# Performance work log

Measured on AMD Instinct MI355X. Metric: run time of the kernel, lower is better.

Reference implementation:

```python
import jax, jax.numpy as jnp
import numpy as np

N_HEAD = 8
DIM_INPUT = 1024
DIM_K = 128
DIM_V = 128
SEG = 512  # segment_length


def setup_inputs() -> dict:
    key = jax.random.key(0)
    ks = jax.random.split(key, 7)
    B, S, D = 4, 8192, DIM_INPUT
    s = 1.0 / np.sqrt(D)
    x = jax.random.normal(ks[0], (B, S, D), jnp.float32)
    wq = jax.random.normal(ks[1], (D, N_HEAD * DIM_K), jnp.float32) * s
    bq = jax.random.normal(ks[2], (N_HEAD * DIM_K,), jnp.float32) * 0.01
    wk = jax.random.normal(ks[3], (D, N_HEAD * DIM_K), jnp.float32) * s
    bk = jax.random.normal(ks[4], (N_HEAD * DIM_K,), jnp.float32) * 0.01
    wv = jax.random.normal(ks[5], (D, N_HEAD * DIM_V), jnp.float32) * s
    bv = jax.random.normal(ks[6], (N_HEAD * DIM_V,), jnp.float32) * 0.01
    beta = jnp.zeros((1,), jnp.float32)  # nn.Parameter(torch.zeros(1))
    return {"x": x, "wq": wq, "bq": bq, "wk": wk, "bk": bk, "wv": wv, "bv": bv, "beta": beta}


def reference(x, wq, bq, wk, bk, wv, bv, beta):
    B, S, D = x.shape
    nseg = S // SEG

    def proj(w, b, d):
        y = x @ w + b  # [B, S, H*d] -- one big GEMM instead of per-segment
        return y.reshape(B, nseg, SEG, N_HEAD, d).transpose(1, 0, 3, 2, 4)  # [nseg, B, H, L, d]

    q = proj(wq, bq, DIM_K)
    k = proj(wk, bk, DIM_K)
    v = proj(wv, bv, DIM_V)

    scale = 1.0 / jnp.sqrt(jnp.asarray(DIM_K, x.dtype))
    bsig = jax.nn.sigmoid(beta)  # (1,), broadcasts

    def step(carry, qkv):
        mem, z = carry  # mem: [B,H,dk,dv], z: [B,H,dk,1]
        qi, ki, vi = qkv  # [B,H,L,dk/dv]
        # memory update (before retrieval, as in source)
        sk = jax.nn.elu(ki) + 1.0
        mem = mem + jnp.einsum('bhlk,bhlv->bhkv', sk, vi)
        z = z + sk.sum(axis=2)[..., None] * SEG
        # memory retrieval
        sq = jax.nn.elu(qi) + 1.0
        a_mem = jnp.einsum('bhlk,bhkv->bhlv', sq, mem) / (
            jnp.einsum('bhlk,bhkd->bhld', sq, z) + 1e-5)
        # local softmax attention
        attn = jax.nn.softmax(jnp.einsum('bhlk,bhmk->bhlm', qi, ki) * scale, axis=-1)
        a_dot = jnp.einsum('bhlm,bhmv->bhlv', attn, vi)
        # head-mean then beta blend
        out = bsig * a_mem.mean(axis=1) + (1.0 - bsig) * a_dot.mean(axis=1)  # [B,L,dv]
        return (mem, z), out

    mem0 = jnp.zeros((B, N_HEAD, DIM_K, DIM_V), x.dtype)
    z0 = jnp.zeros((B, N_HEAD, DIM_K, 1), x.dtype)
    _, outs = jax.lax.scan(step, (mem0, z0), (q, k, v))  # outs: [nseg, B, L, dv]
    return outs.transpose(1, 0, 2, 3).reshape(B, S, DIM_V)
```

## Files before the change

### kernel.cpp

```cpp
#include <hip/hip_runtime.h>
#include <hip/hip_bf16.h>

#define B_    4
#define S_    8192
#define D_    1024
#define H_    8
#define DKV_  128
#define SEG_  512
#define NSEG_ 16
#define BS_   (B_ * S_)

typedef __attribute__((ext_vector_type(8))) short short8;
typedef __attribute__((ext_vector_type(4))) float f32x4;

__device__ inline float bf2f(unsigned short u) {
  unsigned int x = ((unsigned int)u) << 16;
  return __uint_as_float(x);
}
__device__ inline unsigned short f2bf(float f) {
  __hip_bfloat16 h = __float2bfloat16(f);
  return *(unsigned short*)&h;
}
__device__ inline void bf16split(float f, unsigned short& hi, unsigned short& lo) {
  __hip_bfloat16 h = __float2bfloat16(f);
  float hf = __bfloat162float(h);
  __hip_bfloat16 l = __float2bfloat16(f - hf);
  hi = *(unsigned short*)&h;
  lo = *(unsigned short*)&l;
}

__global__ __launch_bounds__(256) void prep_w(
    const float* __restrict__ W, __hip_bfloat16* __restrict__ Whi,
    __hip_bfloat16* __restrict__ Wlo) {
  __shared__ float tile[32][33];
  const int k0 = blockIdx.x * 32, n0 = blockIdx.y * 32;
  const int tx = threadIdx.x & 31, ty = threadIdx.x >> 5;
#pragma unroll
  for (int r = 0; r < 4; ++r) {
    int k = ty + r * 8;
    tile[k][tx] = W[(size_t)(k0 + k) * 1024 + n0 + tx];
  }
  __syncthreads();
#pragma unroll
  for (int r = 0; r < 4; ++r) {
    int n = ty + r * 8;
    float v = tile[tx][n];
    unsigned short hb, lb;
    bf16split(v, hb, lb);
    *(unsigned short*)&Whi[(size_t)(n0 + n) * 1024 + k0 + tx] = hb;
    *(unsigned short*)&Wlo[(size_t)(n0 + n) * 1024 + k0 + tx] = lb;
  }
}

template <int MODE>
__global__ __launch_bounds__(256) void gemm_bf16x3(
    const float* __restrict__ A, const __hip_bfloat16* __restrict__ Bhg,
    const __hip_bfloat16* __restrict__ Blg, const float* __restrict__ bias,
    __hip_bfloat16* __restrict__ Oh, __hip_bfloat16* __restrict__ Ol) {
  __shared__ __hip_bfloat16 Ah[128][40];
  __shared__ __hip_bfloat16 Al[128][40];
  __shared__ __hip_bfloat16 Bh[128][40];
  __shared__ __hip_bfloat16 Bl[128][40];
  const int t = threadIdx.x;
  const int m0 = blockIdx.x * 128, n0 = blockIdx.y * 128;
  const int wave = t >> 6, lane = t & 63;
  const int wm = (wave >> 1) * 64, wn = (wave & 1) * 64;
  const int lr = lane & 15, ks = lane >> 4;

  f32x4 acc[4][4];
#pragma unroll
  for (int i = 0; i < 4; ++i)
#pragma unroll
    for (int j = 0; j < 4; ++j) acc[i][j] = (f32x4){0.f, 0.f, 0.f, 0.f};

  for (int k0 = 0; k0 < 1024; k0 += 32) {
    __syncthreads();
#pragma unroll
    for (int rep = 0; rep < 4; ++rep) {
      int lin = t + rep * 256;
      int row = lin >> 3, kq = (lin & 7) * 4;
      float4 v = *(const float4*)&A[(size_t)(m0 + row) * 1024 + k0 + kq];
      ushort4 hv, lv;
      bf16split(v.x, hv.x, lv.x);
      bf16split(v.y, hv.y, lv.y);
      bf16split(v.z, hv.z, lv.z);
      bf16split(v.w, hv.w, lv.w);
      *(ushort4*)&Ah[row][kq] = hv;
      *(ushort4*)&Al[row][kq] = lv;
    }
#pragma unroll
    for (int rep = 0; rep < 2; ++rep) {
      int lin = t + rep * 256;
      int row = lin >> 2, kq = (lin & 3) * 8;
      *(uint4*)&Bh[row][kq] =
          *(const uint4*)&Bhg[(size_t)(n0 + row) * 1024 + k0 + kq];
      *(uint4*)&Bl[row][kq] =
          *(const uint4*)&Blg[(size_t)(n0 + row) * 1024 + k0 + kq];
    }
    __syncthreads();

    short8 afh[4], afl[4];
#pragma unroll
    for (int fm = 0; fm < 4; ++fm) {
      afh[fm] = *(short8*)&Ah[wm + fm * 16 + lr][ks * 8];
      afl[fm] = *(short8*)&Al[wm + fm * 16 + lr][ks * 8];
    }
#pragma unroll
    for (int fn = 0; fn < 4; ++fn) {
      short8 bfh = *(short8*)&Bh[wn + fn * 16 + lr][ks * 8];
      short8 bfl = *(short8*)&Bl[wn + fn * 16 + lr][ks * 8];
#pragma unroll
      for (int fm = 0; fm < 4; ++fm) {
        acc[fm][fn] = __builtin_amdgcn_mfma_f32_16x16x32_bf16(afh[fm], bfh, acc[fm][fn], 0, 0, 0);
        acc[fm][fn] = __builtin_amdgcn_mfma_f32_16x16x32_bf16(afh[fm], bfl, acc[fm][fn], 0, 0, 0);
        acc[fm][fn] = __builtin_amdgcn_mfma_f32_16x16x32_bf16(afl[fm], bfh, acc[fm][fn], 0, 0, 0);
      }
    }
  }
#pragma unroll
  for (int fn = 0; fn < 4; ++fn) {
    int n = n0 + wn + fn * 16 + lr;
    float bv = bias[n];
#pragma unroll
    for (int fm = 0; fm < 4; ++fm) {
      int mrow = m0 + wm + fm * 16 + ks * 4;
      if (MODE == 0) {
#pragma unroll
        for (int r = 0; r < 4; ++r) {
          float val = acc[fm][fn][r] + bv;
          unsigned short hb, lb;
          bf16split(val, hb, lb);
          *(unsigned short*)&Oh[(size_t)(mrow + r) * 1024 + n] = hb;
          *(unsigned short*)&Ol[(size_t)(mrow + r) * 1024 + n] = lb;
        }
      } else {
        int bb = mrow >> 13, s = mrow & 8191;
        size_t vtix = (((size_t)(bb * 8 + (n >> 7))) * 128 + (n & 127)) * 8192 + s;
        ushort4 pk;
        pk.x = f2bf(acc[fm][fn][0] + bv);
        pk.y = f2bf(acc[fm][fn][1] + bv);
        pk.z = f2bf(acc[fm][fn][2] + bv);
        pk.w = f2bf(acc[fm][fn][3] + bv);
        *(ushort4*)&Oh[vtix] = pk;
      }
    }
  }
}

__global__ __launch_bounds__(256) void seg_kv(
    const __hip_bfloat16* __restrict__ Khp, const __hip_bfloat16* __restrict__ Klp,
    const __hip_bfloat16* __restrict__ VTp, float* __restrict__ MemST,
    float* __restrict__ Zs) {
  __shared__ float sk[16][132];
  __shared__ float svT[128][18];
  const int bx = blockIdx.x;
  const int seg = bx >> 5, bh = bx & 31;
  const int b = bh >> 3, h = bh & 7;
  const int t = threadIdx.x;
  const int tr = t >> 4, tc = t & 15;
  float acc[8][8] = {};
  float zacc = 0.f;
  const size_t rowbase = (size_t)b * S_ + (size_t)seg * SEG_;
  const size_t sbase = (size_t)seg * SEG_;
  const size_t vtbase = (size_t)(b * 8 + h) * 128 * 8192;
  for (int l0 = 0; l0 < SEG_; l0 += 16) {
    __syncthreads();
    {
      int row = t >> 4, oct = t & 15;
      size_t g = (rowbase + l0 + row) * 1024 + h * 128 + oct * 8;
      short8 hv = *(const short8*)&Khp[g];
      short8 lv = *(const short8*)&Klp[g];
#pragma unroll
      for (int e = 0; e < 8; ++e) {
        float kvf = bf2f((unsigned short)hv[e]) + bf2f((unsigned short)lv[e]);
        sk[row][oct * 8 + e] = kvf > 0.f ? kvf + 1.f : __expf(kvf);
      }
      int dv = t >> 1, half = t & 1;
      short8 vv = *(const short8*)&VTp[vtbase + (size_t)dv * 8192 + sbase + l0 + half * 8];
#pragma unroll
      for (int e = 0; e < 8; ++e) svT[dv][half * 8 + e] = bf2f((unsigned short)vv[e]);
    }
    __syncthreads();
#pragma unroll
    for (int l = 0; l < 16; ++l) {
      float a[8], kk[8];
#pragma unroll
      for (int i = 0; i < 8; ++i) a[i] = svT[tr * 8 + i][l];
      *(float4*)&kk[0] = *(const float4*)&sk[l][tc * 8];
      *(float4*)&kk[4] = *(const float4*)&sk[l][tc * 8 + 4];
#pragma unroll
      for (int i = 0; i < 8; ++i)
#pragma unroll
        for (int j = 0; j < 8; ++j)
          acc[i][j] = fmaf(a[i], kk[j], acc[i][j]);
    }
    if (t < 128) {
#pragma unroll
      for (int l = 0; l < 16; ++l) zacc += sk[l][t];
    }
  }
  const size_t base = ((size_t)seg * 32 + bh) * 16384;
#pragma unroll
  for (int i = 0; i < 8; ++i)
#pragma unroll
    for (int j = 0; j < 8; j += 4) {
      float4 o = {acc[i][j], acc[i][j + 1], acc[i][j + 2], acc[i][j + 3]};
      *(float4*)&MemST[base + (size_t)(tr * 8 + i) * 128 + tc * 8 + j] = o;
    }
  if (t < 128) Zs[((size_t)seg * 32 + bh) * 128 + t] = zacc * (float)SEG_;
}

__global__ __launch_bounds__(256) void prefix_scan(
    float* __restrict__ Mem, __hip_bfloat16* __restrict__ MT,
    float* __restrict__ Zs) {
  const int bx = blockIdx.x;
  const int bh = bx & 31;
  const int part = bx >> 5;
  const int t = threadIdx.x;
  for (int jj = 0; jj < 4; ++jj) {
    size_t flat = ((size_t)part * 4 + jj) * 256 + t;
    float run = 0.f;
#pragma unroll
    for (int seg = 0; seg < NSEG_; ++seg) {
      size_t idx = ((size_t)seg * 32 + bh) * 16384 + flat;
      run += Mem[idx];
      Mem[idx] = run;
      *(unsigned short*)&MT[idx] = f2bf(run);
    }
  }
  if (part == 0 && t < 128) {
    float run = 0.f;
#pragma unroll
    for (int seg = 0; seg < NSEG_; ++seg) {
      size_t idx = ((size_t)seg * 32 + bh) * 128 + t;
      run += Zs[idx];
      Zs[idx] = run;
    }
  }
}

__global__ __launch_bounds__(256, 2) void attn_blend_mfma(
    const __hip_bfloat16* __restrict__ Qhp, const __hip_bfloat16* __restrict__ Qlp,
    const __hip_bfloat16* __restrict__ Khp, const __hip_bfloat16* __restrict__ Klp,
    const __hip_bfloat16* __restrict__ VTp, const __hip_bfloat16* __restrict__ MT,
    const float* __restrict__ Zs, const float* __restrict__ beta,
    float* __restrict__ Out) {
  __shared__ __hip_bfloat16 KhS[64][136];
  __shared__ __hip_bfloat16 KlS[64][136];
  __shared__ __hip_bfloat16 VtS[128][72];
  __shared__ __hip_bfloat16 Ps[64][72];
  __shared__ float zl[128];

  const int t = threadIdx.x;
  const int rb = blockIdx.x, seg = blockIdx.y, b = blockIdx.z;
  const int wave = t >> 6, lane = t & 63;
  const int lr = lane & 15, lg = lane >> 4;
  const float scale = 0.08838834764831845f;
  const float bsig = 1.f / (1.f + __expf(-beta[0]));
  const float wmem = bsig * 0.125f, wdot = (1.f - bsig) * 0.125f;

  const size_t segrow = (size_t)b * S_ + (size_t)seg * SEG_;
  const int qrow = rb * 64 + wave * 16 + lr;
  const size_t qbase = (segrow + qrow) * 1024;

  f32x4 accum[8];
#pragma unroll
  for (int v = 0; v < 8; ++v) accum[v] = (f32x4){0.f, 0.f, 0.f, 0.f};

  for (int h = 0; h < H_; ++h) {
    const int bh = b * 8 + h;
    __syncthreads();
    if (t < 128) zl[t] = Zs[((size_t)seg * 32 + bh) * 128 + t];

    short8 ah[4], al[4];
#pragma unroll
    for (int ksv = 0; ksv < 4; ++ksv) {
      size_t off = qbase + h * 128 + lg * 8 + ksv * 32;
      ah[ksv] = *(const short8*)&Qhp[off];
      al[ksv] = *(const short8*)&Qlp[off];
    }

    short8 sqf[4];
    f32x4 sqa[4], sqb[4];
#pragma unroll
    for (int ksv = 0; ksv < 4; ++ksv) {
#pragma unroll
      for (int e = 0; e < 8; ++e) {
        float q = bf2f((unsigned short)ah[ksv][e]) + bf2f((unsigned short)al[ksv][e]);
        float s = q > 0.f ? q + 1.f : __expf(q);
        if (e < 4) sqa[ksv][e] = s; else sqb[ksv][e - 4] = s;
        sqf[ksv][e] = (short)f2bf(s);
      }
    }
    __syncthreads();

    float dnm;
    {
      float part = 0.f;
#pragma unroll
      for (int ksv = 0; ksv < 4; ++ksv) {
        float4 z0 = *(const float4*)&zl[lg * 8 + ksv * 32];
        float4 z1 = *(const float4*)&zl[lg * 8 + ksv * 32 + 4];
        part += sqa[ksv][0] * z0.x + sqa[ksv][1] * z0.y + sqa[ksv][2] * z0.z +
                sqa[ksv][3] * z0.w + sqb[ksv][0] * z1.x + sqb[ksv][1] * z1.y +
                sqb[ksv][2] * z1.z + sqb[ksv][3] * z1.w;
      }
      part += __shfl_xor(part, 16);
      part += __shfl_xor(part, 32);
      dnm = part + 1e-5f;
    }

    f32x4 pm[8];
#pragma unroll
    for (int v = 0; v < 8; ++v) pm[v] = (f32x4){0.f, 0.f, 0.f, 0.f};
    const size_t mtbase = ((size_t)seg * 32 + bh) * 16384;
#pragma unroll 1
    for (int mc = 0; mc < 2; ++mc) {
      if (mc) __syncthreads();
#pragma unroll
      for (int rep = 0; rep < 4; ++rep) {
        int lin = t + rep * 256;
        int dv = lin >> 3, oct = lin & 7;
        *(short8*)&VtS[dv][oct * 8] =
            *(const short8*)&MT[mtbase + (size_t)dv * 128 + mc * 64 + oct * 8];
      }
      __syncthreads();
#pragma unroll
      for (int ks2 = 0; ks2 < 2; ++ks2) {
        short8 af = sqf[mc * 2 + ks2];
#pragma unroll
        for (int vb = 0; vb < 8; ++vb) {
          short8 bf = *(const short8*)&VtS[vb * 16 + lr][ks2 * 32 + lg * 8];
          pm[vb] = __builtin_amdgcn_mfma_f32_16x16x32_bf16(af, bf, pm[vb], 0, 0, 0);
        }
      }
    }
    {
      float cdr[4];
#pragma unroll
      for (int r = 0; r < 4; ++r) cdr[r] = wmem / __shfl(dnm, lg * 4 + r);
#pragma unroll
      for (int vb = 0; vb < 8; ++vb) {
        accum[vb][0] += cdr[0] * pm[vb][0];
        accum[vb][1] += cdr[1] * pm[vb][1];
        accum[vb][2] += cdr[2] * pm[vb][2];
        accum[vb][3] += cdr[3] * pm[vb][3];
      }
    }

    f32x4 o[8];
#pragma unroll
    for (int v = 0; v < 8; ++v) o[v] = (f32x4){0.f, 0.f, 0.f, 0.f};
    float mr_[4] = {-1e30f, -1e30f, -1e30f, -1e30f};
    float lw[4] = {0.f, 0.f, 0.f, 0.f};

#pragma unroll 1
    for (int c = 0; c < 8; ++c) {
      __syncthreads();
#pragma unroll
      for (int rep = 0; rep < 4; ++rep) {
        int lin = t + rep * 256;
        int row = lin >> 4, oct = lin & 15;
        size_t g = (segrow + c * 64 + row) * 1024 + h * 128 + oct * 8;
        *(short8*)&KhS[row][oct * 8] = *(const short8*)&Khp[g];
        *(short8*)&KlS[row][oct * 8] = *(const short8*)&Klp[g];
      }
#pragma unroll
      for (int rep = 0; rep < 4; ++rep) {
        int lin = t + rep * 256;
        int dv = lin >> 3, oct = lin & 7;
        *(short8*)&VtS[dv][oct * 8] =
            *(const short8*)&VTp[((size_t)bh * 128 + dv) * 8192 +
                                 (size_t)seg * 512 + c * 64 + oct * 8];
      }
      __syncthreads();

      f32x4 sblk[4];
#pragma unroll
      for (int kb = 0; kb < 4; ++kb) sblk[kb] = (f32x4){0.f, 0.f, 0.f, 0.f};
#pragma unroll
      for (int kb = 0; kb < 4; ++kb) {
#pragma unroll
        for (int ksv = 0; ksv < 4; ++ksv) {
          short8 bh_ = *(const short8*)&KhS[kb * 16 + lr][ksv * 32 + lg * 8];
          short8 bl_ = *(const short8*)&KlS[kb * 16 + lr][ksv * 32 + lg * 8];
          sblk[kb] = __builtin_amdgcn_mfma_f32_16x16x32_bf16(ah[ksv], bh_, sblk[kb], 0, 0, 0);
          sblk[kb] = __builtin_amdgcn_mfma_f32_16x16x32_bf16(ah[ksv], bl_, sblk[kb], 0, 0, 0);
          sblk[kb] = __builtin_amdgcn_mfma_f32_16x16x32_bf16(al[ksv], bh_, sblk[kb], 0, 0, 0);
        }
      }
      float fsc[4];
#pragma unroll
      for (int r = 0; r < 4; ++r) {
        float s0 = sblk[0][r] * scale, s1 = sblk[1][r] * scale;
        float s2 = sblk[2][r] * scale, s3 = sblk[3][r] * scale;
        float cmax = fmaxf(fmaxf(s0, s1), fmaxf(s2, s3));
        cmax = fmaxf(cmax, __shfl_xor(cmax, 1));
        cmax = fmaxf(cmax, __shfl_xor(cmax, 2));
        cmax = fmaxf(cmax, __shfl_xor(cmax, 4));
        cmax = fmaxf(cmax, __shfl_xor(cmax, 8));
        float mnew = fmaxf(mr_[r], cmax);
        float f = __expf(mr_[r] - mnew);
        float p0 = __expf(s0 - mnew), p1 = __expf(s1 - mnew);
        float p2 = __expf(s2 - mnew), p3 = __expf(s3 - mnew);
        float ps = p0 + p1 + p2 + p3;
        ps += __shfl_xor(ps, 1);
        ps += __shfl_xor(ps, 2);
        ps += __shfl_xor(ps, 4);
        ps += __shfl_xor(ps, 8);
        lw[r] = lw[r] * f + ps;
        mr_[r] = mnew;
        fsc[r] = f;
        int prow = wave * 16 + lg * 4 + r;
        *(unsigned short*)&Ps[prow][lr] = f2bf(p0);
        *(unsigned short*)&Ps[prow][lr + 16] = f2bf(p1);
        *(unsigned short*)&Ps[prow][lr + 32] = f2bf(p2);
        *(unsigned short*)&Ps[prow][lr + 48] = f2bf(p3);
      }
#pragma unroll
      for (int vb = 0; vb < 8; ++vb) {
        o[vb][0] *= fsc[0]; o[vb][1] *= fsc[1];
        o[vb][2] *= fsc[2]; o[vb][3] *= fsc[3];
      }
      short8 pa0 = *(const short8*)&Ps[wave * 16 + lr][lg * 8];
      short8 pa1 = *(const short8*)&Ps[wave * 16 + lr][lg * 8 + 32];
#pragma unroll
      for (int vb = 0; vb < 8; ++vb) {
        short8 b0 = *(const short8*)&VtS[vb * 16 + lr][lg * 8];
        short8 b1 = *(const short8*)&VtS[vb * 16 + lr][lg * 8 + 32];
        o[vb] = __builtin_amdgcn_mfma_f32_16x16x32_bf16(pa0, b0, o[vb], 0, 0, 0);
        o[vb] = __builtin_amdgcn_mfma_f32_16x16x32_bf16(pa1, b1, o[vb], 0, 0, 0);
      }
    }
    {
      float clr[4];
#pragma unroll
      for (int r = 0; r < 4; ++r) clr[r] = wdot / lw[r];
#pragma unroll
      for (int vb = 0; vb < 8; ++vb) {
        accum[vb][0] += clr[0] * o[vb][0];
        accum[vb][1] += clr[1] * o[vb][1];
        accum[vb][2] += clr[2] * o[vb][2];
        accum[vb][3] += clr[3] * o[vb][3];
      }
    }
  }

#pragma unroll
  for (int vb = 0; vb < 8; ++vb)
#pragma unroll
    for (int r = 0; r < 4; ++r) {
      size_t row = segrow + rb * 64 + wave * 16 + lg * 4 + r;
      Out[row * 128 + vb * 16 + lr] = accum[vb][r];
    }
}

extern "C" void kernel_launch(void* const* d_in, const int* in_sizes, int n_in,
                              void* d_out, int out_size, void* d_ws, size_t ws_size,
                              hipStream_t stream) {
  (void)in_sizes; (void)n_in; (void)out_size; (void)ws_size;
  const float* x    = (const float*)d_in[0];
  const float* wq   = (const float*)d_in[1];
  const float* bq   = (const float*)d_in[2];
  const float* wk   = (const float*)d_in[3];
  const float* bk   = (const float*)d_in[4];
  const float* wv   = (const float*)d_in[5];
  const float* bv   = (const float*)d_in[6];
  const float* beta = (const float*)d_in[7];
  float* Out = (float*)d_out;

  const size_t PL = (size_t)BS_ * 1024;
  __hip_bfloat16* Qhp = (__hip_bfloat16*)d_ws;
  __hip_bfloat16* Qlp = Qhp + PL;
  __hip_bfloat16* Khp = Qlp + PL;
  __hip_bfloat16* Klp = Khp + PL;
  __hip_bfloat16* VTp = Klp + PL;
  __hip_bfloat16* MT  = VTp + PL;
  float* MemST = (float*)(MT + (size_t)NSEG_ * 32 * 16384);
  float* Zs = MemST + (size_t)NSEG_ * 32 * 16384;
  __hip_bfloat16* Wt = (__hip_bfloat16*)(Zs + (size_t)NSEG_ * 32 * 128);
  const size_t WSZ = (size_t)1024 * 1024;
  __hip_bfloat16* Wqh = Wt;
  __hip_bfloat16* Wql = Wqh + WSZ;
  __hip_bfloat16* Wkh = Wql + WSZ;
  __hip_bfloat16* Wkl = Wkh + WSZ;
  __hip_bfloat16* Wvh = Wkl + WSZ;
  __hip_bfloat16* Wvl = Wvh + WSZ;

  dim3 b256(256);
  dim3 gp(32, 32);
  prep_w<<<gp, b256, 0, stream>>>(wq, Wqh, Wql);
  prep_w<<<gp, b256, 0, stream>>>(wk, Wkh, Wkl);
  prep_w<<<gp, b256, 0, stream>>>(wv, Wvh, Wvl);

  dim3 gg(256, 8);
  gemm_bf16x3<0><<<gg, b256, 0, stream>>>(x, Wqh, Wql, bq, Qhp, Qlp);
  gemm_bf16x3<0><<<gg, b256, 0, stream>>>(x, Wkh, Wkl, bk, Khp, Klp);
  gemm_bf16x3<1><<<gg, b256, 0, stream>>>(x, Wvh, Wvl, bv, VTp, nullptr);

  seg_kv<<<512, b256, 0, stream>>>(Khp, Klp, VTp, MemST, Zs);
  prefix_scan<<<512, b256, 0, stream>>>(MemST, MT, Zs);
  attn_blend_mfma<<<dim3(8, 16, 4), b256, 0, stream>>>(
      Qhp, Qlp, Khp, Klp, VTp, MT, Zs, beta, Out);
}
```

Measured before the change: 1.729 ms.

## Pre-split x into bf16 hi/lo once, remap grids, fix seg_kv V layout

Adds a split_x kernel that converts x to bf16 hi/lo planes once, so the three projection GEMMs load pre-split bf16 instead of each re-reading fp32 x and re-splitting it. The path is used only when the workspace is large enough, with the split planes aliased into the region later used for MT/MemST/Zs. GEMM and attention launches move to 1D grids with an m-major tile order, which changes the order blocks are scheduled in and could affect cache reuse. seg_kv now stores V transposed in shared memory so each thread reads contiguous float4 vectors instead of strided scalars.

After: 1.686 ms. 1.03x faster.

```diff
diff --git a/kernel.cpp b/kernel.cpp
--- a/kernel.cpp
+++ b/kernel.cpp
@@ -52,17 +52,37 @@
   }
 }
 
-template <int MODE>
+__global__ __launch_bounds__(256) void split_x(
+    const float* __restrict__ X, __hip_bfloat16* __restrict__ Ah,
+    __hip_bfloat16* __restrict__ Al) {
+  const size_t n4 = (size_t)BS_ * 1024 / 4;
+  for (size_t idx = (size_t)blockIdx.x * 256 + threadIdx.x; idx < n4;
+       idx += (size_t)gridDim.x * 256) {
+    float4 v = *(const float4*)&X[idx * 4];
+    ushort4 hv, lv;
+    bf16split(v.x, hv.x, lv.x);
+    bf16split(v.y, hv.y, lv.y);
+    bf16split(v.z, hv.z, lv.z);
+    bf16split(v.w, hv.w, lv.w);
+    *(ushort4*)&Ah[idx * 4] = hv;
+    *(ushort4*)&Al[idx * 4] = lv;
+  }
+}
+
+template <int MODE, int PRE>
 __global__ __launch_bounds__(256) void gemm_bf16x3(
-    const float* __restrict__ A, const __hip_bfloat16* __restrict__ Bhg,
-    const __hip_bfloat16* __restrict__ Blg, const float* __restrict__ bias,
+    const float* __restrict__ Af, const __hip_bfloat16* __restrict__ Ahp,
+    const __hip_bfloat16* __restrict__ Alp,
+    const __hip_bfloat16* __restrict__ Bhg, const __hip_bfloat16* __restrict__ Blg,
+    const float* __restrict__ bias,
     __hip_bfloat16* __restrict__ Oh, __hip_bfloat16* __restrict__ Ol) {
   __shared__ __hip_bfloat16 Ah[128][40];
   __shared__ __hip_bfloat16 Al[128][40];
   __shared__ __hip_bfloat16 Bh[128][40];
   __shared__ __hip_bfloat16 Bl[128][40];
   const int t = threadIdx.x;
-  const int m0 = blockIdx.x * 128, n0 = blockIdx.y * 128;
+  const int wgid = blockIdx.x;
+  const int m0 = (wgid >> 3) * 128, n0 = (wgid & 7) * 128;
   const int wave = t >> 6, lane = t & 63;
   const int wm = (wave >> 1) * 64, wn = (wave & 1) * 64;
   const int lr = lane & 15, ks = lane >> 4;
@@ -75,18 +95,30 @@
 
   for (int k0 = 0; k0 < 1024; k0 += 32) {
     __syncthreads();
-#pragma unroll
-    for (int rep = 0; rep < 4; ++rep) {
-      int lin = t + rep * 256;
-      int row = lin >> 3, kq = (lin & 7) * 4;
-      float4 v = *(const float4*)&A[(size_t)(m0 + row) * 1024 + k0 + kq];
-      ushort4 hv, lv;
-      bf16split(v.x, hv.x, lv.x);
-      bf16split(v.y, hv.y, lv.y);
-      bf16split(v.z, hv.z, lv.z);
-      bf16split(v.w, hv.w, lv.w);
-      *(ushort4*)&Ah[row][kq] = hv;
-      *(ushort4*)&Al[row][kq] = lv;
+    if (PRE) {
+#pragma unroll
+      for (int rep = 0; rep < 2; ++rep) {
+        int lin = t + rep * 256;
+        int row = lin >> 2, kq = (lin & 3) * 8;
+        *(uint4*)&Ah[row][kq] =
+            *(const uint4*)&Ahp[(size_t)(m0 + row) * 1024 + k0 + kq];
+        *(uint4*)&Al[row][kq] =
+            *(const uint4*)&Alp[(size_t)(m0 + row) * 1024 + k0 + kq];
+      }
+    } else {
+#pragma unroll
+      for (int rep = 0; rep < 4; ++rep) {
+        int lin = t + rep * 256;
+        int row = lin >> 3, kq = (lin & 7) * 4;
+        float4 v = *(const float4*)&Af[(size_t)(m0 + row) * 1024 + k0 + kq];
+        ushort4 hv, lv;
+        bf16split(v.x, hv.x, lv.x);
+        bf16split(v.y, hv.y, lv.y);
+        bf16split(v.z, hv.z, lv.z);
+        bf16split(v.w, hv.w, lv.w);
+        *(ushort4*)&Ah[row][kq] = hv;
+        *(ushort4*)&Al[row][kq] = lv;
+      }
     }
 #pragma unroll
     for (int rep = 0; rep < 2; ++rep) {
@@ -152,7 +184,7 @@
     const __hip_bfloat16* __restrict__ VTp, float* __restrict__ MemST,
     float* __restrict__ Zs) {
   __shared__ float sk[16][132];
-  __shared__ float svT[128][18];
+  __shared__ float sv[16][132];
   const int bx = blockIdx.x;
   const int seg = bx >> 5, bh = bx & 31;
   const int b = bh >> 3, h = bh & 7;
@@ -178,14 +210,14 @@
       int dv = t >> 1, half = t & 1;
       short8 vv = *(const short8*)&VTp[vtbase + (size_t)dv * 8192 + sbase + l0 + half * 8];
 #pragma unroll
-      for (int e = 0; e < 8; ++e) svT[dv][half * 8 + e] = bf2f((unsigned short)vv[e]);
+      for (int e = 0; e < 8; ++e) sv[half * 8 + e][dv] = bf2f((unsigned short)vv[e]);
     }
     __syncthreads();
 #pragma unroll
     for (int l = 0; l < 16; ++l) {
       float a[8], kk[8];
-#pragma unroll
-      for (int i = 0; i < 8; ++i) a[i] = svT[tr * 8 + i][l];
+      *(float4*)&a[0] = *(const float4*)&sv[l][tr * 8];
+      *(float4*)&a[4] = *(const float4*)&sv[l][tr * 8 + 4];
       *(float4*)&kk[0] = *(const float4*)&sk[l][tc * 8];
       *(float4*)&kk[4] = *(const float4*)&sk[l][tc * 8 + 4];
 #pragma unroll
@@ -252,7 +284,10 @@
   __shared__ float zl[128];
 
   const int t = threadIdx.x;
-  const int rb = blockIdx.x, seg = blockIdx.y, b = blockIdx.z;
+  const int wgid = blockIdx.x;
+  const int rb = wgid >> 6;
+  const int segb = wgid & 63;
+  const int seg = segb & 15, b = segb >> 4;
   const int wave = t >> 6, lane = t & 63;
   const int lr = lane & 15, lg = lane >> 4;
   const float scale = 0.08838834764831845f;
@@ -458,7 +493,7 @@
 extern "C" void kernel_launch(void* const* d_in, const int* in_sizes, int n_in,
                               void* d_out, int out_size, void* d_ws, size_t ws_size,
                               hipStream_t stream) {
-  (void)in_sizes; (void)n_in; (void)out_size; (void)ws_size;
+  (void)in_sizes; (void)n_in; (void)out_size;
   const float* x    = (const float*)d_in[0];
   const float* wq   = (const float*)d_in[1];
   const float* bq   = (const float*)d_in[2];
@@ -470,22 +505,34 @@
   float* Out = (float*)d_out;
 
   const size_t PL = (size_t)BS_ * 1024;
-  __hip_bfloat16* Qhp = (__hip_bfloat16*)d_ws;
-  __hip_bfloat16* Qlp = Qhp + PL;
-  __hip_bfloat16* Khp = Qlp + PL;
-  __hip_bfloat16* Klp = Khp + PL;
-  __hip_bfloat16* VTp = Klp + PL;
-  __hip_bfloat16* MT  = VTp + PL;
-  float* MemST = (float*)(MT + (size_t)NSEG_ * 32 * 16384);
-  float* Zs = MemST + (size_t)NSEG_ * 32 * 16384;
-  __hip_bfloat16* Wt = (__hip_bfloat16*)(Zs + (size_t)NSEG_ * 32 * 128);
+  const size_t PLb = PL * 2;
+  const size_t MEMN = (size_t)NSEG_ * 32 * 16384;
+  char* p = (char*)d_ws;
+  __hip_bfloat16* Qhp = (__hip_bfloat16*)p;          p += PLb;
+  __hip_bfloat16* Qlp = (__hip_bfloat16*)p;          p += PLb;
+  __hip_bfloat16* Khp = (__hip_bfloat16*)p;          p += PLb;
+  __hip_bfloat16* Klp = (__hip_bfloat16*)p;          p += PLb;
+  __hip_bfloat16* VTp = (__hip_bfloat16*)p;          p += PLb;
+  char* r1 = p;
+  __hip_bfloat16* MT  = (__hip_bfloat16*)r1;
+  float* MemST = (float*)(r1 + MEMN * 2);
+  float* Zs    = (float*)(r1 + MEMN * 2 + MEMN * 4);
+  const size_t aliasB = MEMN * 2 + MEMN * 4 + (size_t)NSEG_ * 32 * 128 * 4;
+  __hip_bfloat16* Ahp = (__hip_bfloat16*)r1;
+  __hip_bfloat16* Alp = Ahp + PL;
   const size_t WSZ = (size_t)1024 * 1024;
+  const size_t need_split  = 5 * PLb + 2 * PLb + 6 * WSZ * 2;
+  bool use_split = (ws_size >= need_split);
+  size_t r1sz = use_split ? (2 * PLb) : aliasB;
+  if (!use_split && aliasB < 2 * PLb) r1sz = aliasB;
+  __hip_bfloat16* Wt = (__hip_bfloat16*)(r1 + (use_split ? 2 * PLb : aliasB));
   __hip_bfloat16* Wqh = Wt;
   __hip_bfloat16* Wql = Wqh + WSZ;
   __hip_bfloat16* Wkh = Wql + WSZ;
   __hip_bfloat16* Wkl = Wkh + WSZ;
   __hip_bfloat16* Wvh = Wkl + WSZ;
   __hip_bfloat16* Wvl = Wvh + WSZ;
+  (void)r1sz;
 
   dim3 b256(256);
   dim3 gp(32, 32);
@@ -493,13 +540,19 @@
   prep_w<<<gp, b256, 0, stream>>>(wk, Wkh, Wkl);
   prep_w<<<gp, b256, 0, stream>>>(wv, Wvh, Wvl);
 
-  dim3 gg(256, 8);
-  gemm_bf16x3<0><<<gg, b256, 0, stream>>>(x, Wqh, Wql, bq, Qhp, Qlp);
-  gemm_bf16x3<0><<<gg, b256, 0, stream>>>(x, Wkh, Wkl, bk, Khp, Klp);
-  gemm_bf16x3<1><<<gg, b256, 0, stream>>>(x, Wvh, Wvl, bv, VTp, nullptr);
+  if (use_split) {
+    split_x<<<2048, b256, 0, stream>>>(x, Ahp, Alp);
+    gemm_bf16x3<0, 1><<<2048, b256, 0, stream>>>(x, Ahp, Alp, Wqh, Wql, bq, Qhp, Qlp);
+    gemm_bf16x3<0, 1><<<2048, b256, 0, stream>>>(x, Ahp, Alp, Wkh, Wkl, bk, Khp, Klp);
+    gemm_bf16x3<1, 1><<<2048, b256, 0, stream>>>(x, Ahp, Alp, Wvh, Wvl, bv, VTp, nullptr);
+  } else {
+    gemm_bf16x3<0, 0><<<2048, b256, 0, stream>>>(x, nullptr, nullptr, Wqh, Wql, bq, Qhp, Qlp);
+    gemm_bf16x3<0, 0><<<2048, b256, 0, stream>>>(x, nullptr, nullptr, Wkh, Wkl, bk, Khp, Klp);
+    gemm_bf16x3<1, 0><<<2048, b256, 0, stream>>>(x, nullptr, nullptr, Wvh, Wvl, bv, VTp, nullptr);
+  }
 
   seg_kv<<<512, b256, 0, stream>>>(Khp, Klp, VTp, MemST, Zs);
   prefix_scan<<<512, b256, 0, stream>>>(MemST, MT, Zs);
-  attn_blend_mfma<<<dim3(8, 16, 4), b256, 0, stream>>>(
+  attn_blend_mfma<<<512, b256, 0, stream>>>(
       Qhp, Qlp, Khp, Klp, VTp, MT, Zs, beta, Out);
 }
```
